# Kernel optimization log

Measured on AMD Instinct MI355X. Metric: run time of the kernel, lower is better.

## Reference

```python
import jax, jax.numpy as jnp
import numpy as np

TEMP = 0.5  # temperature_f from init


def setup_inputs() -> dict:
    key = jax.random.key(0)
    k1, k2, k3 = jax.random.split(key, 3)
    B, d = 4096, 128
    h_i = jax.random.normal(k1, (B, d), dtype=jnp.float32)
    h_j = jax.random.normal(k2, (B, d), dtype=jnp.float32)
    S = jax.random.uniform(k3, (B, B), dtype=jnp.float32)
    return {"h_i": h_i, "h_j": h_j, "S": S}


def reference(h_i, h_j, S):
    B = h_i.shape[0]
    N = 2 * B
    h = jnp.concatenate([h_i, h_j], axis=0)                 # [N, d]
    sim = jnp.matmul(h, h.T) / TEMP                          # [N, N]
    # S_2 = 1 - (S**2).repeat(2,2); sim1 = sim * S_2
    S2 = 1.0 - jnp.tile(S * S, (2, 2))                       # [N, N]
    sim1 = sim * S2
    # positives: diag(sim, +B) and diag(sim, -B)
    idx = jnp.arange(B)
    pos = jnp.concatenate([sim[idx, idx + B], sim[idx + B, idx]])  # [N]
    # negatives mask: exclude diagonal and the positive-pair positions
    i = jnp.arange(N)[:, None]
    j = jnp.arange(N)[None, :]
    neg_mask = ~((i == j) | (j == (i + B) % N))              # [N, N], N-2 True per row
    neg = jnp.where(neg_mask, sim1, -jnp.inf)                # masked entries drop out of logsumexp
    # CrossEntropy(label=0, reduction='sum') over logits=[pos, negatives]:
    # loss_n = logsumexp(logits_n) - pos_n  (order of negatives is irrelevant)
    logits = jnp.concatenate([pos[:, None], neg], axis=1)    # [N, N-1] effective
    lse = jax.nn.logsumexp(logits, axis=1)
    loss = jnp.sum(lse - pos) / N
    return loss
```

## Files before the change

kernel.cpp:

```cpp
#include <hip/hip_runtime.h>
#include <hip/hip_bf16.h>

#define B_ROWS 4096
#define NN     8192
#define DD     128
#define NTRI   2080
#define CSHIFT 128.0f

typedef __attribute__((ext_vector_type(8))) short s8v;
typedef __attribute__((ext_vector_type(4))) float f4v;
typedef __attribute__((ext_vector_type(2))) float f2v;
typedef unsigned int u32;
typedef unsigned short u16;
typedef unsigned char u8;

static constexpr float SCALE_H = 1.6986436f;
static constexpr float SCALE2  = 2.8853900818f;
static constexpr float LN2     = 0.6931471805599453f;
static constexpr float INV255  = 1.0f / 255.0f;

__device__ __forceinline__ float fast_exp2(float x) {
#if __has_builtin(__builtin_amdgcn_exp2f)
    return __builtin_amdgcn_exp2f(x);
#else
    return exp2f(x);
#endif
}

__device__ __forceinline__ u8 s2m_pack8(float x, bool msk) {
    float s2 = msk ? 0.f : 1.f - x * x;
    return (u8)(s2 * 255.f + 0.5f);
}

__device__ __forceinline__ u16 f2bf(float x) {
    union { __hip_bfloat16 h; u16 u; } cv;
    cv.h = __float2bfloat16(x);
    return cv.u;
}

__device__ __forceinline__ float bf2f(u16 u) {
    return __uint_as_float(((u32)u) << 16);
}

typedef __attribute__((address_space(1))) const u32 gu32;
typedef __attribute__((address_space(3))) u32 lu32;
__device__ __forceinline__ void gload_lds16(const void* g, void* l) {
    __builtin_amdgcn_global_load_lds((gu32*)g, (lu32*)l, 16, 0, 0);
}

__global__ void hpos_kernel(const float* __restrict__ hi, const float* __restrict__ hj,
                            __hip_bfloat16* __restrict__ hb, float* __restrict__ pos2) {
    int w = threadIdx.x >> 6, l = threadIdx.x & 63;
    int row = blockIdx.x * 4 + w;
    f2v a = ((const f2v*)(hi + (size_t)row * DD))[l];
    f2v b = ((const f2v*)(hj + (size_t)row * DD))[l];
    float d = a[0] * b[0] + a[1] * b[1];
    #pragma unroll
    for (int off = 32; off; off >>= 1) d += __shfl_xor(d, off, 64);
    if (l == 0) pos2[row] = SCALE2 * d;
    union { ushort2 u2; __hip_bfloat16 h[2]; } ua, ub;
    ua.h[0] = __float2bfloat16(a[0] * SCALE_H);
    ua.h[1] = __float2bfloat16(a[1] * SCALE_H);
    ub.h[0] = __float2bfloat16(b[0] * SCALE_H);
    ub.h[1] = __float2bfloat16(b[1] * SCALE_H);
    ((ushort2*)(hb + (size_t)row * DD))[l] = ua.u2;
    ((ushort2*)(hb + (size_t)(row + B_ROWS) * DD))[l] = ub.u2;
}

__global__ __launch_bounds__(512, 4)
void main_kernel(const __hip_bfloat16* __restrict__ hb, const float* __restrict__ S,
                 u16* __restrict__ ssr, u16* __restrict__ ssc) {
    __shared__ short ldsB[128][128];
    __shared__ __align__(16) u8 sAu[64 * 64];
    __shared__ __align__(16) u8 sBtu[64 * 64];

    const int orig = blockIdx.x;
    const int bid  = (orig & 7) * (NTRI / 8) + (orig >> 3);
    int j = (int)((sqrtf(8.0f * (float)bid + 1.0f) - 1.0f) * 0.5f);
    while (((j + 1) * (j + 2)) / 2 <= bid) ++j;
    while ((j * (j + 1)) / 2 > bid) --j;
    const int i = bid - (j * (j + 1)) / 2;
    const bool diag = (i == j);

    const int tid = threadIdx.x;
    const int l  = tid & 63;
    const int w  = tid >> 6;
    const int wm = w >> 1, wn = w & 1;
    const int lc = l & 15;
    const int lk = l >> 4;
    const int r64 = i * 64, c64 = j * 64;

    const s8v* hb8 = (const s8v*)hb;

    #pragma unroll
    for (int i2 = 0; i2 < 4; i2++) {
        const int rowb = w * 16 + i2 * 4;
        const int lrw  = rowb + lk;
        const int grow = c64 + ((lrw < 64) ? lrw : (lrw - 64 + B_ROWS));
        const int sc16 = lc ^ (lrw & 7);
        gload_lds16((const char*)hb + ((size_t)grow << 8) + (sc16 << 4),
                    (char*)&ldsB[rowb][0]);
    }

    {
        const int prr = tid >> 3;
        const int pc8 = (tid & 7) * 8;
        const float* gA = S + (size_t)(r64 + prr) * B_ROWS + c64 + pc8;
        const float* gB = S + (size_t)(c64 + prr) * B_ROWS + r64 + pc8;
        f4v a0 = ((const f4v*)gA)[0], a1 = ((const f4v*)gA)[1];
        f4v b0 = ((const f4v*)gB)[0], b1 = ((const f4v*)gB)[1];
        union { u8 c[8]; uint2 v; } qa;
        u8 qb[8];
        #pragma unroll
        for (int e = 0; e < 4; e++) {
            qa.c[e]     = s2m_pack8(a0[e], diag && (pc8 + e     == prr));
            qa.c[e + 4] = s2m_pack8(a1[e], diag && (pc8 + 4 + e == prr));
            qb[e]     = s2m_pack8(b0[e], false);
            qb[e + 4] = s2m_pack8(b1[e], false);
        }
        *(uint2*)&sAu[prr * 64 + pc8] = qa.v;
        #pragma unroll
        for (int e = 0; e < 8; e++)
            sBtu[(pc8 + e) * 64 + prr] = qb[e];
    }

    s8v afr[2][4];
    #pragma unroll
    for (int fm = 0; fm < 2; fm++) {
        int ar = (r64 + wm * 16 + lc) + fm * B_ROWS;
        #pragma unroll
        for (int kk = 0; kk < 4; kk++)
            afr[fm][kk] = hb8[ar * 16 + kk * 4 + lk];
    }
    __syncthreads();

    const char* bp[4];
    {
        const char* bb = (const char*)ldsB + (wn * 32 + lc) * 256;
        #pragma unroll
        for (int kk = 0; kk < 4; kk++)
            bp[kk] = bb + (((kk * 4 + lk) ^ (lc & 7)) << 4);
    }
    f4v acc[2][2][2];
    #pragma unroll
    for (int fm = 0; fm < 2; fm++)
        #pragma unroll
        for (int fh = 0; fh < 2; fh++)
            #pragma unroll
            for (int cg = 0; cg < 2; cg++) acc[fm][fh][cg] = f4v{0.f, 0.f, 0.f, 0.f};
    #pragma unroll
    for (int kk = 0; kk < 4; kk++) {
        #pragma unroll
        for (int fh = 0; fh < 2; fh++)
            #pragma unroll
            for (int cg = 0; cg < 2; cg++) {
                s8v bf = *(const s8v*)(bp[kk] + fh * 16384 + cg * 4096);
                acc[0][fh][cg] = __builtin_amdgcn_mfma_f32_16x16x32_bf16(
                    afr[0][kk], bf, acc[0][fh][cg], 0, 0, 0);
                acc[1][fh][cg] = __builtin_amdgcn_mfma_f32_16x16x32_bf16(
                    afr[1][kk], bf, acc[1][fh][cg], 0, 0, 0);
            }
    }

    float rsum[2][4], csum[2][2];
    #pragma unroll
    for (int fm = 0; fm < 2; fm++)
        #pragma unroll
        for (int r = 0; r < 4; r++) rsum[fm][r] = 0.f;
    csum[0][0] = csum[0][1] = csum[1][0] = csum[1][1] = 0.f;

    #pragma unroll
    for (int r = 0; r < 4; r++) {
        const int rr = wm * 16 + lk * 4 + r;
        #pragma unroll
        for (int cg = 0; cg < 2; cg++) {
            const int cc = wn * 32 + cg * 16 + lc;
            const float s2a = (float)sAu[rr * 64 + cc] * INV255;
            const float s2b = (float)sBtu[rr * 64 + cc] * INV255;
            #pragma unroll
            for (int fm = 0; fm < 2; fm++)
                #pragma unroll
                for (int fh = 0; fh < 2; fh++) {
                    const float a = acc[fm][fh][cg][r];
                    rsum[fm][r]  += fast_exp2(fmaf(a, s2a, -CSHIFT));
                    csum[fh][cg] += fast_exp2(fmaf(a, s2b, -CSHIFT));
                }
        }
    }

    #pragma unroll
    for (int fm = 0; fm < 2; fm++) {
        #pragma unroll
        for (int r = 0; r < 4; r++) {
            float ss = rsum[fm][r];
            #pragma unroll
            for (int off = 1; off < 16; off <<= 1) ss += __shfl_xor(ss, off, 64);
            if (lc == 0) {
                int rho = wm * 16 + lk * 4 + r;
                ssr[(size_t)(j * 2 + wn) * NN + (r64 + rho + fm * B_ROWS)] = f2bf(ss);
            }
        }
    }
    #pragma unroll
    for (int fh = 0; fh < 2; fh++) {
        #pragma unroll
        for (int cg = 0; cg < 2; cg++) {
            float ss = csum[fh][cg];
            ss += __shfl_xor(ss, 16, 64);
            ss += __shfl_xor(ss, 32, 64);
            if (l < 16) {
                int cc = wn * 32 + cg * 16 + lc;
                ssc[(size_t)(i * 4 + wm) * NN + (c64 + cc + fh * B_ROWS)] = f2bf(ss);
            }
        }
    }
}

__global__ __launch_bounds__(256)
void reduce_kernel(const u16* __restrict__ ssr, const u16* __restrict__ ssc,
                   const float* __restrict__ pos2, float* __restrict__ partial) {
    __shared__ float red[256];
    const int r = threadIdx.x & 31;
    const int s = threadIdx.x >> 5;
    const int n = blockIdx.x * 32 + r;
    const int it = (n & (B_ROWS - 1)) >> 6;
    float ssum = 0.f;
    for (int sp = 2 * it + s; sp < 128; sp += 8)
        ssum += bf2f(ssr[(size_t)sp * NN + n]);
    for (int sp = s; sp < 4 * it; sp += 8)
        ssum += bf2f(ssc[(size_t)sp * NN + n]);
    red[threadIdx.x] = ssum;
    __syncthreads();
    if (threadIdx.x < 32) {
        float t = 0.f;
        #pragma unroll
        for (int k = 0; k < 8; k++) t += red[threadIdx.x + 32 * k];
        float p = pos2[n & (B_ROWS - 1)];
        float Ssum = t + fast_exp2(p - CSHIFT);
        red[threadIdx.x] = (CSHIFT + log2f(Ssum)) - p;
    }
    __syncthreads();
    if (threadIdx.x == 0) {
        float acc = 0.f;
        #pragma unroll
        for (int k = 0; k < 32; k++) acc += red[k];
        partial[blockIdx.x] = acc;
    }
}

__global__ __launch_bounds__(256)
void final_kernel(const float* __restrict__ partial, float* __restrict__ out) {
    __shared__ float red[256];
    red[threadIdx.x] = partial[threadIdx.x];
    __syncthreads();
    for (int st = 128; st; st >>= 1) {
        if (threadIdx.x < st) red[threadIdx.x] += red[threadIdx.x + st];
        __syncthreads();
    }
    if (threadIdx.x == 0) out[0] = red[0] * (LN2 / (float)NN);
}

extern "C" void kernel_launch(void* const* d_in, const int* in_sizes, int n_in,
                              void* d_out, int out_size, void* d_ws, size_t ws_size,
                              hipStream_t stream) {
    (void)in_sizes; (void)n_in; (void)out_size; (void)ws_size;
    const float* hi = (const float*)d_in[0];
    const float* hj = (const float*)d_in[1];
    const float* S  = (const float*)d_in[2];

    char* ws = (char*)d_ws;
    __hip_bfloat16* hb = (__hip_bfloat16*)ws;
    float* pos2   = (float*)(ws + 2097152);
    u16*   ssr    = (u16*)(ws + 2097152 + 16384);
    u16*   ssc    = (u16*)(ws + 2097152 + 16384 + 2097152);
    float* partial= (float*)(ws + 2097152 + 16384 + 2097152 + 4194304);

    hpos_kernel<<<1024, 256, 0, stream>>>(hi, hj, hb, pos2);
    main_kernel<<<NTRI, 512, 0, stream>>>(hb, S, ssr, ssc);
    reduce_kernel<<<256, 256, 0, stream>>>(ssr, ssc, pos2, partial);
    final_kernel<<<1, 256, 0, stream>>>(partial, (float*)d_out);
}
```

Baseline: 51.23 us.

## Make main kernel persistent with double-buffered prefetch of next tile

The main kernel goes from one block per triangular tile to 512 persistent blocks, each working through a contiguous range of tiles. While the current tile is computed, the next tile's B rows (async global-to-LDS) and S values are prefetched into a second LDS buffer. This hides load latency and amortizes launch and setup cost. In exchange it doubles LDS use, which may reduce occupancy, and uneven tile counts per block can leave load imbalance.

```diff
diff --git a/kernel.cpp b/kernel.cpp
--- a/kernel.cpp
+++ b/kernel.cpp
@@ -5,6 +5,7 @@
 #define NN     8192
 #define DD     128
 #define NTRI   2080
+#define NB     512
 #define CSHIFT 128.0f
 
 typedef __attribute__((ext_vector_type(8))) short s8v;
@@ -47,6 +48,14 @@
 __device__ __forceinline__ void gload_lds16(const void* g, void* l) {
     __builtin_amdgcn_global_load_lds((gu32*)g, (lu32*)l, 16, 0, 0);
 }
+
+#define DECODE(BID, I, J) do {                                         \
+    int _b = (BID);                                                    \
+    int _j = (int)((sqrtf(8.f * (float)_b + 1.f) - 1.f) * 0.5f);       \
+    while (((_j + 1) * (_j + 2)) / 2 <= _b) ++_j;                      \
+    while ((_j * (_j + 1)) / 2 > _b) --_j;                             \
+    (J) = _j; (I) = _b - (_j * (_j + 1)) / 2;                          \
+} while (0)
 
 __global__ void hpos_kernel(const float* __restrict__ hi, const float* __restrict__ hj,
                             __hip_bfloat16* __restrict__ hb, float* __restrict__ pos2) {
@@ -70,17 +79,14 @@
 __global__ __launch_bounds__(512, 4)
 void main_kernel(const __hip_bfloat16* __restrict__ hb, const float* __restrict__ S,
                  u16* __restrict__ ssr, u16* __restrict__ ssc) {
-    __shared__ short ldsB[128][128];
-    __shared__ __align__(16) u8 sAu[64 * 64];
-    __shared__ __align__(16) u8 sBtu[64 * 64];
+    __shared__ short ldsB[2][128][128];
+    __shared__ __align__(16) u8 sAu[2][4096];
+    __shared__ __align__(16) u8 sBtu[2][4096];
 
     const int orig = blockIdx.x;
-    const int bid  = (orig & 7) * (NTRI / 8) + (orig >> 3);
-    int j = (int)((sqrtf(8.0f * (float)bid + 1.0f) - 1.0f) * 0.5f);
-    while (((j + 1) * (j + 2)) / 2 <= bid) ++j;
-    while ((j * (j + 1)) / 2 > bid) --j;
-    const int i = bid - (j * (j + 1)) / 2;
-    const bool diag = (i == j);
+    const int rb   = (orig & 7) * 64 + (orig >> 3);
+    const int start = (rb * NTRI) >> 9;
+    const int cnt   = (((rb + 1) * NTRI) >> 9) - start;
 
     const int tid = threadIdx.x;
     const int l  = tid & 63;
@@ -88,132 +94,165 @@
     const int wm = w >> 1, wn = w & 1;
     const int lc = l & 15;
     const int lk = l >> 4;
-    const int r64 = i * 64, c64 = j * 64;
+    const int prr = tid >> 3;
+    const int pc8 = (tid & 7) * 8;
 
     const s8v* hb8 = (const s8v*)hb;
 
-    #pragma unroll
-    for (int i2 = 0; i2 < 4; i2++) {
-        const int rowb = w * 16 + i2 * 4;
-        const int lrw  = rowb + lk;
-        const int grow = c64 + ((lrw < 64) ? lrw : (lrw - 64 + B_ROWS));
-        const int sc16 = lc ^ (lrw & 7);
-        gload_lds16((const char*)hb + ((size_t)grow << 8) + (sc16 << 4),
-                    (char*)&ldsB[rowb][0]);
-    }
-
+#define BSTAGE(P, J) do {                                                         \
+    _Pragma("unroll")                                                             \
+    for (int i2 = 0; i2 < 4; i2++) {                                              \
+        const int rowb = w * 16 + i2 * 4;                                         \
+        const int lrw  = rowb + lk;                         \
+        const int grow = (J) * 64 + ((lrw < 64) ? lrw : (lrw - 64 + B_ROWS));     \
+        const int sc16 = lc ^ (lrw & 7);                  \
+        gload_lds16((const char*)hb + ((size_t)grow << 8) + (sc16 << 4),          \
+                    (char*)&ldsB[P][rowb][0]);                                    \
+    }                                                                             \
+} while (0)
+
+#define SLOAD(I, J, A0, A1, B0, B1) do {                                          \
+    const float* _gA = S + (size_t)((I) * 64 + prr) * B_ROWS + (J) * 64 + pc8;    \
+    const float* _gB = S + (size_t)((J) * 64 + prr) * B_ROWS + (I) * 64 + pc8;    \
+    A0 = ((const f4v*)_gA)[0]; A1 = ((const f4v*)_gA)[1];                         \
+    B0 = ((const f4v*)_gB)[0]; B1 = ((const f4v*)_gB)[1];                         \
+} while (0)
+
+#define SPACK(P, I, J, A0, A1, B0, B1) do {                                       \
+    const bool _dg = ((I) == (J));                                                \
+    union { u8 c[8]; uint2 v; } _qa;                                              \
+    u8 _qb[8];                                                                    \
+    _Pragma("unroll")                                                             \
+    for (int e = 0; e < 4; e++) {                                                 \
+        _qa.c[e]     = s2m_pack8(A0[e], _dg && (pc8 + e     == prr));             \
+        _qa.c[e + 4] = s2m_pack8(A1[e], _dg && (pc8 + 4 + e == prr));             \
+        _qb[e]     = s2m_pack8(B0[e], false);                                     \
+        _qb[e + 4] = s2m_pack8(B1[e], false);                                     \
+    }                                                                             \
+    *(uint2*)&sAu[P][prr * 64 + pc8] = _qa.v;                                     \
+    _Pragma("unroll")                                                             \
+    for (int e = 0; e < 8; e++)                                                   \
+        sBtu[P][(pc8 + e) * 64 + prr] = _qb[e];                                   \
+} while (0)
+
+    int ci, cj;
+    DECODE(start, ci, cj);
+    BSTAGE(0, cj);
     {
-        const int prr = tid >> 3;
-        const int pc8 = (tid & 7) * 8;
-        const float* gA = S + (size_t)(r64 + prr) * B_ROWS + c64 + pc8;
-        const float* gB = S + (size_t)(c64 + prr) * B_ROWS + r64 + pc8;
-        f4v a0 = ((const f4v*)gA)[0], a1 = ((const f4v*)gA)[1];
-        f4v b0 = ((const f4v*)gB)[0], b1 = ((const f4v*)gB)[1];
-        union { u8 c[8]; uint2 v; } qa;
-        u8 qb[8];
-        #pragma unroll
-        for (int e = 0; e < 4; e++) {
-            qa.c[e]     = s2m_pack8(a0[e], diag && (pc8 + e     == prr));
-            qa.c[e + 4] = s2m_pack8(a1[e], diag && (pc8 + 4 + e == prr));
-            qb[e]     = s2m_pack8(b0[e], false);
-            qb[e + 4] = s2m_pack8(b1[e], false);
-        }
-        *(uint2*)&sAu[prr * 64 + pc8] = qa.v;
-        #pragma unroll
-        for (int e = 0; e < 8; e++)
-            sBtu[(pc8 + e) * 64 + prr] = qb[e];
-    }
-
-    s8v afr[2][4];
-    #pragma unroll
-    for (int fm = 0; fm < 2; fm++) {
-        int ar = (r64 + wm * 16 + lc) + fm * B_ROWS;
-        #pragma unroll
-        for (int kk = 0; kk < 4; kk++)
-            afr[fm][kk] = hb8[ar * 16 + kk * 4 + lk];
-    }
-    __syncthreads();
-
-    const char* bp[4];
-    {
-        const char* bb = (const char*)ldsB + (wn * 32 + lc) * 256;
-        #pragma unroll
-        for (int kk = 0; kk < 4; kk++)
-            bp[kk] = bb + (((kk * 4 + lk) ^ (lc & 7)) << 4);
-    }
-    f4v acc[2][2][2];
-    #pragma unroll
-    for (int fm = 0; fm < 2; fm++)
-        #pragma unroll
-        for (int fh = 0; fh < 2; fh++)
-            #pragma unroll
-            for (int cg = 0; cg < 2; cg++) acc[fm][fh][cg] = f4v{0.f, 0.f, 0.f, 0.f};
-    #pragma unroll
-    for (int kk = 0; kk < 4; kk++) {
-        #pragma unroll
-        for (int fh = 0; fh < 2; fh++)
+        f4v a0, a1, b0, b1;
+        SLOAD(ci, cj, a0, a1, b0, b1);
+        SPACK(0, ci, cj, a0, a1, b0, b1);
+    }
+
+    for (int t = 0; t < cnt; ++t) {
+        const int p = t & 1;
+        __syncthreads();
+
+        const bool hn = (t + 1 < cnt);
+        int ni = ci, nj = cj;
+        f4v na0, na1, nb0, nb1;
+        if (hn) {
+            DECODE(start + t + 1, ni, nj);
+            BSTAGE(1 - p, nj);
+            SLOAD(ni, nj, na0, na1, nb0, nb1);
+        }
+
+        s8v afr[2][4];
+        #pragma unroll
+        for (int fm = 0; fm < 2; fm++) {
+            int ar = (ci * 64 + wm * 16 + lc) + fm * B_ROWS;
+            #pragma unroll
+            for (int kk = 0; kk < 4; kk++)
+                afr[fm][kk] = hb8[ar * 16 + kk * 4 + lk];
+        }
+
+        const char* bp[4];
+        {
+            const char* bb = (const char*)&ldsB[p][0][0] + (wn * 32 + lc) * 256;
+            #pragma unroll
+            for (int kk = 0; kk < 4; kk++)
+                bp[kk] = bb + (((kk * 4 + lk) ^ (lc & 7)) << 4);
+        }
+        f4v acc[2][2][2];
+        #pragma unroll
+        for (int fm = 0; fm < 2; fm++)
+            #pragma unroll
+            for (int fh = 0; fh < 2; fh++)
+                #pragma unroll
+                for (int cg = 0; cg < 2; cg++) acc[fm][fh][cg] = f4v{0.f, 0.f, 0.f, 0.f};
+        #pragma unroll
+        for (int kk = 0; kk < 4; kk++) {
+            #pragma unroll
+            for (int fh = 0; fh < 2; fh++)
+                #pragma unroll
+                for (int cg = 0; cg < 2; cg++) {
+                    s8v bf = *(const s8v*)(bp[kk] + fh * 16384 + cg * 4096);
+                    acc[0][fh][cg] = __builtin_amdgcn_mfma_f32_16x16x32_bf16(
+                        afr[0][kk], bf, acc[0][fh][cg], 0, 0, 0);
+                    acc[1][fh][cg] = __builtin_amdgcn_mfma_f32_16x16x32_bf16(
+                        afr[1][kk], bf, acc[1][fh][cg], 0, 0, 0);
+                }
+        }
+
+        float rsum[2][4], csum[2][2];
+        #pragma unroll
+        for (int fm = 0; fm < 2; fm++)
+            #pragma unroll
+            for (int r = 0; r < 4; r++) rsum[fm][r] = 0.f;
+        csum[0][0] = csum[0][1] = csum[1][0] = csum[1][1] = 0.f;
+
+        #pragma unroll
+        for (int r = 0; r < 4; r++) {
+            const int rr = wm * 16 + lk * 4 + r;
             #pragma unroll
             for (int cg = 0; cg < 2; cg++) {
-                s8v bf = *(const s8v*)(bp[kk] + fh * 16384 + cg * 4096);
-                acc[0][fh][cg] = __builtin_amdgcn_mfma_f32_16x16x32_bf16(
-                    afr[0][kk], bf, acc[0][fh][cg], 0, 0, 0);
-                acc[1][fh][cg] = __builtin_amdgcn_mfma_f32_16x16x32_bf16(
-                    afr[1][kk], bf, acc[1][fh][cg], 0, 0, 0);
+                const int cc = wn * 32 + cg * 16 + lc;
+                const float s2a = (float)sAu[p][rr * 64 + cc] * INV255;
+                const float s2b = (float)sBtu[p][rr * 64 + cc] * INV255;
+                #pragma unroll
+                for (int fm = 0; fm < 2; fm++)
+                    #pragma unroll
+                    for (int fh = 0; fh < 2; fh++) {
+                        const float a = acc[fm][fh][cg][r];
+                        rsum[fm][r]  += fast_exp2(fmaf(a, s2a, -CSHIFT));
+                        csum[fh][cg] += fast_exp2(fmaf(a, s2b, -CSHIFT));
+                    }
             }
-    }
-
-    float rsum[2][4], csum[2][2];
-    #pragma unroll
-    for (int fm = 0; fm < 2; fm++)
-        #pragma unroll
-        for (int r = 0; r < 4; r++) rsum[fm][r] = 0.f;
-    csum[0][0] = csum[0][1] = csum[1][0] = csum[1][1] = 0.f;
-
-    #pragma unroll
-    for (int r = 0; r < 4; r++) {
-        const int rr = wm * 16 + lk * 4 + r;
-        #pragma unroll
-        for (int cg = 0; cg < 2; cg++) {
-            const int cc = wn * 32 + cg * 16 + lc;
-            const float s2a = (float)sAu[rr * 64 + cc] * INV255;
-            const float s2b = (float)sBtu[rr * 64 + cc] * INV255;
-            #pragma unroll
-            for (int fm = 0; fm < 2; fm++)
+        }
+
+        if (hn) SPACK(1 - p, ni, nj, na0, na1, nb0, nb1);
+
+        #pragma unroll
+        for (int fm = 0; fm < 2; fm++) {
+            #pragma unroll
+            for (int r = 0; r < 4; r++) {
+                float ss = rsum[fm][r];
                 #pragma unroll
-                for (int fh = 0; fh < 2; fh++) {
-                    const float a = acc[fm][fh][cg][r];
-                    rsum[fm][r]  += fast_exp2(fmaf(a, s2a, -CSHIFT));
-                    csum[fh][cg] += fast_exp2(fmaf(a, s2b, -CSHIFT));
+                for (int off = 1; off < 16; off <<= 1) ss += __shfl_xor(ss, off, 64);
+                if (lc == 0) {
+                    int rho = wm * 16 + lk * 4 + r;
+                    ssr[(size_t)(cj * 2 + wn) * NN + (ci * 64 + rho + fm * B_ROWS)] = f2bf(ss);
                 }
-        }
-    }
-
-    #pragma unroll
-    for (int fm = 0; fm < 2; fm++) {
-        #pragma unroll
-        for (int r = 0; r < 4; r++) {
-            float ss = rsum[fm][r];
-            #pragma unroll
-            for (int off = 1; off < 16; off <<= 1) ss += __shfl_xor(ss, off, 64);
-            if (lc == 0) {
-                int rho = wm * 16 + lk * 4 + r;
-                ssr[(size_t)(j * 2 + wn) * NN + (r64 + rho + fm * B_ROWS)] = f2bf(ss);
             }
         }
-    }
-    #pragma unroll
-    for (int fh = 0; fh < 2; fh++) {
-        #pragma unroll
-        for (int cg = 0; cg < 2; cg++) {
-            float ss = csum[fh][cg];
-            ss += __shfl_xor(ss, 16, 64);
-            ss += __shfl_xor(ss, 32, 64);
-            if (l < 16) {
-                int cc = wn * 32 + cg * 16 + lc;
-                ssc[(size_t)(i * 4 + wm) * NN + (c64 + cc + fh * B_ROWS)] = f2bf(ss);
+        #pragma unroll
+        for (int fh = 0; fh < 2; fh++) {
+            #pragma unroll
+            for (int cg = 0; cg < 2; cg++) {
+                float ss = csum[fh][cg];
+                ss += __shfl_xor(ss, 16, 64);
+                ss += __shfl_xor(ss, 32, 64);
+                if (l < 16) {
+                    int cc = wn * 32 + cg * 16 + lc;
+                    ssc[(size_t)(ci * 4 + wm) * NN + (cj * 64 + cc + fh * B_ROWS)] = f2bf(ss);
+                }
             }
         }
-    }
+        ci = ni; cj = nj;
+    }
+#undef BSTAGE
+#undef SLOAD
+#undef SPACK
 }
 
 __global__ __launch_bounds__(256)
@@ -276,7 +315,7 @@
     float* partial= (float*)(ws + 2097152 + 16384 + 2097152 + 4194304);
 
     hpos_kernel<<<1024, 256, 0, stream>>>(hi, hj, hb, pos2);
-    main_kernel<<<NTRI, 512, 0, stream>>>(hb, S, ssr, ssc);
+    main_kernel<<<NB, 512, 0, stream>>>(hb, S, ssr, ssc);
     reduce_kernel<<<256, 256, 0, stream>>>(ssr, ssc, pos2, partial);
     final_kernel<<<1, 256, 0, stream>>>(partial, (float*)d_out);
 }
```

Result: slower. 59.01 us (+15.2%).
